# Kernel optimization log

Measured on AMD Instinct MI355X. Metric: run time of the kernel, lower is better.

The kernel has to match this reference:

```python
import jax, jax.numpy as jnp
import numpy as np

B, S, D = 2, 4096, 1024
H, DK = 16, 64          # heads, QK feature dim per head
DV = D // H             # output features per head = 64
QKV_OUT = (2 * DK + DV) * H  # 3072


def setup_inputs() -> dict:
    key = jax.random.key(0)
    k1, k2, k3, k4, k5 = jax.random.split(key, 5)
    x = jax.random.normal(k1, (B, S, D), dtype=jnp.float32)
    Wqkv = jax.random.normal(k2, (D, QKV_OUT), dtype=jnp.float32) * (1.0 / np.sqrt(D))
    bqkv = jnp.zeros((QKV_OUT,), dtype=jnp.float32)
    Wproj = jax.random.normal(k3, (D, D), dtype=jnp.float32) * (1.0 / np.sqrt(D))
    bproj = jnp.zeros((D,), dtype=jnp.float32)
    return {"x": x, "Wqkv": Wqkv, "bqkv": bqkv, "Wproj": Wproj, "bproj": bproj}


def reference(x, Wqkv, bqkv, Wproj, bproj):
    # QKV projection: [B,S,(2*DK+DV)*H]
    qkv = x @ Wqkv + bqkv
    q_len = DK * H
    Q = qkv[:, :, :q_len].reshape(B, S, H, DK).transpose(0, 2, 1, 3)        # [B,H,S,DK]
    K = qkv[:, :, q_len:2 * q_len].reshape(B, S, H, DK).transpose(0, 2, 1, 3)
    V = qkv[:, :, 2 * q_len:].reshape(B, S, H, DV).transpose(0, 2, 1, 3)    # [B,H,S,DV]

    scores = jnp.einsum("bhqd,bhkd->bhqk", Q, K) * (1.0 / np.sqrt(DK))
    # Faithful to source: causal mask is tril(ones) with zeros -> -inf,
    # i.e. +1.0 is ADDED on allowed positions (harmless constant shift per row).
    tril = jnp.tril(jnp.ones((S, S), dtype=jnp.float32))
    mask = jnp.where(tril == 0, -jnp.inf, tril)
    scores = scores + mask
    attn = jax.nn.softmax(scores, axis=-1)  # dropout disabled (p=0 / eval)

    out = jnp.einsum("bhqk,bhkd->bhqd", attn, V)            # [B,H,S,DV]
    out = out.transpose(0, 2, 1, 3).reshape(B, S, H * DV)   # [B,S,D]
    return out @ Wproj + bproj
```

## Files before the change

kernel.cpp:

```cpp
#include <hip/hip_runtime.h>
#include <stdint.h>


typedef __bf16 bf16x8 __attribute__((ext_vector_type(8)));
typedef float f32x4 __attribute__((ext_vector_type(4)));
typedef unsigned short u16x8 __attribute__((ext_vector_type(8)));
typedef unsigned short u16x4 __attribute__((ext_vector_type(4)));
typedef unsigned int u32x4 __attribute__((ext_vector_type(4)));

__device__ __forceinline__ unsigned short f2bf(float f) {
  unsigned u = __builtin_bit_cast(unsigned, f);
  u += 0x7FFFu + ((u >> 16) & 1u);
  return (unsigned short)(u >> 16);
}

__device__ __forceinline__ float fast_exp2(float x) {
#if __has_builtin(__builtin_amdgcn_exp2f)
  return __builtin_amdgcn_exp2f(x);
#else
  return exp2f(x);
#endif
}

__device__ __forceinline__ void gload16(const void* g, void* l) {
  __builtin_amdgcn_global_load_lds(
      (__attribute__((address_space(1))) unsigned int*)(uintptr_t)g,
      (__attribute__((address_space(3))) unsigned int*)(unsigned int)(uintptr_t)l,
      16, 0, 0);
}

__global__ void k_cvt_bf16(const float* __restrict__ in,
                           unsigned short* __restrict__ out, int n8) {
  int i = blockIdx.x * blockDim.x + threadIdx.x;
  if (i >= n8) return;
  const float4* p = reinterpret_cast<const float4*>(in) + (size_t)i * 2;
  float4 a = p[0], b = p[1];
  u16x8 o;
  o[0] = f2bf(a.x); o[1] = f2bf(a.y); o[2] = f2bf(a.z); o[3] = f2bf(a.w);
  o[4] = f2bf(b.x); o[5] = f2bf(b.y); o[6] = f2bf(b.z); o[7] = f2bf(b.w);
  *(reinterpret_cast<u16x8*>(out) + i) = o;
}

__global__ void k_transcvt(const float* __restrict__ in,
                           unsigned short* __restrict__ out, int K, int N) {
  __shared__ float tile[32][33];
  int tk0 = blockIdx.y << 5, tn0 = blockIdx.x << 5;
  int t = threadIdx.x;
  int r = t >> 3, c4 = (t & 7) << 2;
  float4 v = *reinterpret_cast<const float4*>(&in[(size_t)(tk0 + r) * N + tn0 + c4]);
  tile[r][c4 + 0] = v.x; tile[r][c4 + 1] = v.y;
  tile[r][c4 + 2] = v.z; tile[r][c4 + 3] = v.w;
  __syncthreads();
  u16x4 o;
  o[0] = f2bf(tile[c4 + 0][r]); o[1] = f2bf(tile[c4 + 1][r]);
  o[2] = f2bf(tile[c4 + 2][r]); o[3] = f2bf(tile[c4 + 3][r]);
  *reinterpret_cast<u16x4*>(&out[(size_t)(tn0 + r) * K + tk0 + c4]) = o;
}

__device__ __forceinline__ void gemm_core(
    const unsigned short* __restrict__ A, const unsigned short* __restrict__ Bt,
    unsigned short* Al, unsigned short* Bl, int m0, int n0, f32x4 acc[4][4]) {
  const int t = threadIdx.x;
  const int lane = t & 63;
  const int w = t >> 6;
  const int wr = w >> 1, wc = w & 1;
  const int l15 = lane & 15, l4 = lane >> 4;

  const int c0 = t, c1 = t + 256;
  const int r0 = c0 >> 2, s0 = ((c0 & 3) << 3) ^ (((r0 >> 1) & 3) << 3);
  const int r1 = c1 >> 2, s1 = ((c1 & 3) << 3) ^ (((r1 >> 1) & 3) << 3);
  const size_t ga0 = (size_t)(m0 + r0) * 1024 + s0;
  const size_t ga1 = (size_t)(m0 + r1) * 1024 + s1;
  const size_t gb0 = (size_t)(n0 + r0) * 1024 + s0;
  const size_t gb1 = (size_t)(n0 + r1) * 1024 + s1;

  int aidx[4], bidx[4];
#pragma unroll
  for (int m = 0; m < 4; ++m) {
    int row = wr * 64 + m * 16 + l15;
    aidx[m] = row * 32 + ((l4 * 8) ^ (((row >> 1) & 3) << 3));
    row = wc * 64 + m * 16 + l15;
    bidx[m] = row * 32 + ((l4 * 8) ^ (((row >> 1) & 3) << 3));
  }

  for (int kk = 0; kk < 1024; kk += 32) {
    __syncthreads();
    gload16(A + ga0 + kk, Al + c0 * 8);
    gload16(A + ga1 + kk, Al + c1 * 8);
    gload16(Bt + gb0 + kk, Bl + c0 * 8);
    gload16(Bt + gb1 + kk, Bl + c1 * 8);
    __syncthreads();
    bf16x8 af[4], bfr[4];
#pragma unroll
    for (int m = 0; m < 4; ++m)
      af[m] = *reinterpret_cast<const bf16x8*>(Al + aidx[m]);
#pragma unroll
    for (int n = 0; n < 4; ++n)
      bfr[n] = *reinterpret_cast<const bf16x8*>(Bl + bidx[n]);
#pragma unroll
    for (int m = 0; m < 4; ++m)
#pragma unroll
      for (int n = 0; n < 4; ++n)
        acc[m][n] = __builtin_amdgcn_mfma_f32_16x16x32_bf16(af[m], bfr[n],
                                                            acc[m][n], 0, 0, 0);
  }
}

__global__ __launch_bounds__(256) void k_gemm_qkv(
    const unsigned short* __restrict__ A, const unsigned short* __restrict__ Bt,
    const float* __restrict__ bias, unsigned short* __restrict__ Qb,
    unsigned short* __restrict__ Kb, unsigned short* __restrict__ VTb) {
  __shared__ unsigned short Al[128 * 32];
  __shared__ unsigned short Bl[128 * 32];
  const int lane = threadIdx.x & 63, w = threadIdx.x >> 6;
  const int wr = w >> 1, wc = w & 1;
  const int l15 = lane & 15, l4 = lane >> 4;
  const int m0 = blockIdx.y << 7, n0 = blockIdx.x << 7;
  const float C1 = 0.18033688011112043f;

  f32x4 acc[4][4] = {};
  gemm_core(A, Bt, Al, Bl, m0, n0, acc);

#pragma unroll
  for (int m = 0; m < 4; ++m) {
#pragma unroll
    for (int n = 0; n < 4; ++n) {
#pragma unroll
      for (int j = 0; j < 4; ++j) {
        int row = m0 + wr * 64 + m * 16 + l4 * 4 + j;
        int col = n0 + wc * 64 + n * 16 + l15;
        float v = acc[m][n][j] + bias[col];
        int b = row >> 12, s = row & 4095;
        if (col < 1024) {
          int hh = col >> 6, d = col & 63;
          Qb[((size_t)(b * 16 + hh) * 4096 + s) * 64 + d] = f2bf(v * C1);
        } else if (col < 2048) {
          int cc = col - 1024; int hh = cc >> 6, d = cc & 63;
          Kb[((size_t)(b * 16 + hh) * 4096 + s) * 64 + d] = f2bf(v);
        } else {
          int cc = col - 2048; int hh = cc >> 6, d = cc & 63;
          VTb[((size_t)(b * 16 + hh) * 64 + d) * 4096 + s] = f2bf(v);
        }
      }
    }
  }
}

__global__ __launch_bounds__(256) void k_gemm_proj(
    const unsigned short* __restrict__ A, const unsigned short* __restrict__ Bt,
    const float* __restrict__ bias, float* __restrict__ out) {
  __shared__ unsigned short Al[128 * 32];
  __shared__ unsigned short Bl[128 * 32];
  const int lane = threadIdx.x & 63, w = threadIdx.x >> 6;
  const int wr = w >> 1, wc = w & 1;
  const int l15 = lane & 15, l4 = lane >> 4;
  const int m0 = blockIdx.y << 7, n0 = blockIdx.x << 7;

  f32x4 acc[4][4] = {};
  gemm_core(A, Bt, Al, Bl, m0, n0, acc);

#pragma unroll
  for (int m = 0; m < 4; ++m) {
#pragma unroll
    for (int n = 0; n < 4; ++n) {
#pragma unroll
      for (int j = 0; j < 4; ++j) {
        int row = m0 + wr * 64 + m * 16 + l4 * 4 + j;
        int col = n0 + wc * 64 + n * 16 + l15;
        out[(size_t)row * 1024 + col] = acc[m][n][j] + bias[col];
      }
    }
  }
}

__global__ __launch_bounds__(256, 4) void k_attn(
    const unsigned short* __restrict__ Qb, const unsigned short* __restrict__ Kb,
    const unsigned short* __restrict__ VTb, unsigned short* __restrict__ Ob) {
  __shared__ unsigned short Kl[2][64 * 64];
  __shared__ unsigned short Vl[2][64 * 64];
  const int t = threadIdx.x;
  const int lane = t & 63, w = t >> 6;
  const int l15 = lane & 15, l4 = lane >> 4;
  const int idx = blockIdx.x;
  const int qt = 31 - (idx >> 5);
  const int bh = idx & 31;
  const size_t qkbase = (size_t)bh * 4096 * 64;
  const size_t vbase = (size_t)bh * 64 * 4096;
  const int b = bh >> 4, hh = bh & 15;
  const int wrow0 = qt * 128 + w * 32;
  const int nt = 2 * qt + 2;

  const int c0 = t, c1 = t + 256;
  const int kr0 = c0 >> 3, ks0 = ((c0 & 7) << 3) ^ ((kr0 & 7) << 3);
  const int kr1 = c1 >> 3, ks1 = ((c1 & 7) << 3) ^ ((kr1 & 7) << 3);

#define STAGE(bufi, jt)                                                             \
  do {                                                                              \
    gload16(Kb + qkbase + (size_t)((jt) * 64 + kr0) * 64 + ks0, &Kl[bufi][c0 * 8]); \
    gload16(Kb + qkbase + (size_t)((jt) * 64 + kr1) * 64 + ks1, &Kl[bufi][c1 * 8]); \
    gload16(VTb + vbase + (size_t)kr0 * 4096 + (jt) * 64 + ks0, &Vl[bufi][c0 * 8]); \
    gload16(VTb + vbase + (size_t)kr1 * 4096 + (jt) * 64 + ks1, &Vl[bufi][c1 * 8]); \
  } while (0)

  bf16x8 qf[2][2];
#pragma unroll
  for (int m = 0; m < 2; ++m)
#pragma unroll
    for (int kk = 0; kk < 2; ++kk)
      qf[m][kk] = *reinterpret_cast<const bf16x8*>(
          &Qb[qkbase + (size_t)(wrow0 + m * 16 + l15) * 64 + kk * 32 + l4 * 8]);

  f32x4 oacc[2][4] = {};
  float lsum[2] = {};

  STAGE(0, 0);
  asm volatile("s_waitcnt vmcnt(0)" ::: "memory");
  __builtin_amdgcn_s_barrier();

  for (int j = 0; j < nt; ++j) {
    const int cur = j & 1;
    if (j + 1 < nt) STAGE(cur ^ 1, j + 1);

    const int jk0 = j * 64;
    const bool active = (jk0 <= wrow0 + 31);
    const bool needmask = active && (jk0 + 63 > wrow0);

    if (active) {
#pragma unroll
      for (int h = 0; h < 2; ++h) {
        f32x4 sch[2][2] = {};
        __builtin_amdgcn_s_setprio(1);
#pragma unroll
        for (int nn = 0; nn < 2; ++nn) {
          int krow = (h * 2 + nn) * 16 + l15;
#pragma unroll
          for (int kk = 0; kk < 2; ++kk) {
            int kcol = (kk * 32 + l4 * 8) ^ ((krow & 7) << 3);
            bf16x8 kfr = *reinterpret_cast<const bf16x8*>(&Kl[cur][krow * 64 + kcol]);
#pragma unroll
            for (int m = 0; m < 2; ++m)
              sch[m][nn] = __builtin_amdgcn_mfma_f32_16x16x32_bf16(
                  kfr, qf[m][kk], sch[m][nn], 0, 0, 0);
          }
        }
        __builtin_amdgcn_s_setprio(0);

        bf16x8 pa[2];
#pragma unroll
        for (int m = 0; m < 2; ++m) {
#pragma unroll
          for (int nn = 0; nn < 2; ++nn)
#pragma unroll
            for (int r = 0; r < 4; ++r)
              sch[m][nn][r] = fast_exp2(sch[m][nn][r]);
          if (needmask) {
            const int qg = wrow0 + m * 16 + l15;
#pragma unroll
            for (int nn = 0; nn < 2; ++nn) {
              const int kb = jk0 + (h * 2 + nn) * 16 + l4 * 4;
#pragma unroll
              for (int r = 0; r < 4; ++r)
                if (kb + r > qg) sch[m][nn][r] = 0.f;
            }
          }
#pragma unroll
          for (int nn = 0; nn < 2; ++nn)
#pragma unroll
            for (int r = 0; r < 4; ++r)
              lsum[m] += sch[m][nn][r];

          unsigned A0, A1, B0, B1;
          asm("v_cvt_pk_bf16_f32 %0, %1, %2"
              : "=v"(A0) : "v"(sch[m][0][0]), "v"(sch[m][0][1]));
          asm("v_cvt_pk_bf16_f32 %0, %1, %2"
              : "=v"(A1) : "v"(sch[m][0][2]), "v"(sch[m][0][3]));
          asm("v_cvt_pk_bf16_f32 %0, %1, %2"
              : "=v"(B0) : "v"(sch[m][1][0]), "v"(sch[m][1][1]));
          asm("v_cvt_pk_bf16_f32 %0, %1, %2"
              : "=v"(B1) : "v"(sch[m][1][2]), "v"(sch[m][1][3]));
          asm("v_permlane32_swap_b32 %0, %1" : "+v"(A0), "+v"(B0));
          asm("v_permlane16_swap_b32 %0, %1" : "+v"(A0), "+v"(B0));
          asm("v_permlane32_swap_b32 %0, %1" : "+v"(A1), "+v"(B1));
          asm("v_permlane16_swap_b32 %0, %1" : "+v"(A1), "+v"(B1));
          u32x4 pw;
          pw[0] = A0; pw[1] = A1; pw[2] = B0; pw[3] = B1;
          pa[m] = __builtin_bit_cast(bf16x8, pw);
        }

        __builtin_amdgcn_s_setprio(1);
#pragma unroll
        for (int nn2 = 0; nn2 < 4; ++nn2) {
          int vr = nn2 * 16 + l15;
          int vc = (h * 32 + l4 * 8) ^ ((vr & 7) << 3);
          bf16x8 vf = *reinterpret_cast<const bf16x8*>(&Vl[cur][vr * 64 + vc]);
          oacc[0][nn2] = __builtin_amdgcn_mfma_f32_16x16x32_bf16(
              pa[0], vf, oacc[0][nn2], 0, 0, 0);
          oacc[1][nn2] = __builtin_amdgcn_mfma_f32_16x16x32_bf16(
              pa[1], vf, oacc[1][nn2], 0, 0, 0);
        }
        __builtin_amdgcn_s_setprio(0);
      }
    }

    asm volatile("s_waitcnt vmcnt(0)" ::: "memory");
    __builtin_amdgcn_s_barrier();
  }
#undef STAGE

#pragma unroll
  for (int m = 0; m < 2; ++m) {
    lsum[m] += __shfl_xor(lsum[m], 16);
    lsum[m] += __shfl_xor(lsum[m], 32);
  }
#pragma unroll
  for (int m = 0; m < 2; ++m)
#pragma unroll
    for (int jj = 0; jj < 4; ++jj) {
      float inv = 1.0f / __shfl(lsum[m], l4 * 4 + jj);
      int srow = wrow0 + m * 16 + l4 * 4 + jj;
#pragma unroll
      for (int nn = 0; nn < 4; ++nn) {
        int col = hh * 64 + nn * 16 + l15;
        Ob[((size_t)(b * 4096 + srow)) * 1024 + col] =
            __builtin_bit_cast(unsigned short, (__bf16)(oacc[m][nn][jj] * inv));
      }
    }
}

extern "C" void kernel_launch(void* const* d_in, const int* in_sizes, int n_in,
                              void* d_out, int out_size, void* d_ws, size_t ws_size,
                              hipStream_t stream) {
  const float* x = (const float*)d_in[0];
  const float* Wqkv = (const float*)d_in[1];
  const float* bqkv = (const float*)d_in[2];
  const float* Wproj = (const float*)d_in[3];
  const float* bproj = (const float*)d_in[4];

  char* ws = (char*)d_ws;
  unsigned short* xb  = (unsigned short*)(ws);
  unsigned short* Wqb = (unsigned short*)(ws + 16777216);
  unsigned short* Wpb = (unsigned short*)(ws + 23068672);
  unsigned short* Qb  = (unsigned short*)(ws + 25165824);
  unsigned short* Kb  = (unsigned short*)(ws + 41943040);
  unsigned short* VTb = (unsigned short*)(ws + 58720256);
  unsigned short* Ob  = (unsigned short*)(ws + 75497472);

  k_cvt_bf16<<<dim3(8388608 / 8 / 256), dim3(256), 0, stream>>>(x, xb, 8388608 / 8);
  k_transcvt<<<dim3(3072 / 32, 1024 / 32), dim3(256), 0, stream>>>(Wqkv, Wqb, 1024, 3072);
  k_transcvt<<<dim3(1024 / 32, 1024 / 32), dim3(256), 0, stream>>>(Wproj, Wpb, 1024, 1024);
  k_gemm_qkv<<<dim3(3072 / 128, 8192 / 128), dim3(256), 0, stream>>>(xb, Wqb, bqkv, Qb, Kb, VTb);
  k_attn<<<dim3(1024), dim3(256), 0, stream>>>(Qb, Kb, VTb, Ob);
  k_gemm_proj<<<dim3(1024 / 128, 8192 / 128), dim3(256), 0, stream>>>(Ob, Wpb, bproj, (float*)d_out);
}
```

Baseline: 222.2 us.

## Replace QKV GEMM with 256x256 tile, 4-stage LDS ring pipeline

The QKV projection GEMM moves from 128x128 tiles with 256 threads and a single-buffered LDS stage to 256x256 tiles with 512 threads and a 4-deep LDS ring. The ring prefetches three K-steps ahead using manual vmcnt waits and barriers, and the kernel raises wave priority around the MFMA bursts. The goal is more data reuse per tile and hiding global-load latency behind compute. The costs are 64KB of LDS per block, higher register pressure from 8x4 accumulators, and only 384 blocks, which may fill the CUs unevenly.

```diff
diff --git a/kernel.cpp b/kernel.cpp
--- a/kernel.cpp
+++ b/kernel.cpp
@@ -57,6 +57,139 @@
   *reinterpret_cast<u16x4*>(&out[(size_t)(tn0 + r) * K + tk0 + c4]) = o;
 }
 
+__global__ __launch_bounds__(512, 2) void k_gemm_qkv256(
+    const unsigned short* __restrict__ A, const unsigned short* __restrict__ Bt,
+    const float* __restrict__ bias, unsigned short* __restrict__ Qb,
+    unsigned short* __restrict__ Kb, unsigned short* __restrict__ VTb) {
+  __shared__ unsigned short Aring[4][8192];
+  __shared__ unsigned short Bring[4][8192];
+  const int t = threadIdx.x;
+  const int lane = t & 63;
+  const int w = t >> 6;
+  const int wr = w >> 2, wc = w & 3;
+  const int l15 = lane & 15, l4 = lane >> 4;
+  const int m0 = blockIdx.y << 8, n0 = blockIdx.x << 8;
+
+  const int ca0 = t, ca1 = t + 512;
+  const size_t gA0 = (size_t)(m0 + (ca0 & 255)) * 1024 + ((ca0 >> 8) << 3);
+  const size_t gA1 = (size_t)(m0 + (ca1 & 255)) * 1024 + ((ca1 >> 8) << 3);
+  const size_t gB0 = (size_t)(n0 + (ca0 & 255)) * 1024 + ((ca0 >> 8) << 3);
+  const size_t gB1 = (size_t)(n0 + (ca1 & 255)) * 1024 + ((ca1 >> 8) << 3);
+
+  const int abase = l4 * 2048 + (wr * 128 + l15) * 8;
+  const int bbase = l4 * 2048 + (wc * 64 + l15) * 8;
+
+  f32x4 acc[8][4] = {};
+
+  auto stageU = [&](int g) {
+    const int s = g & 3;
+    const int k = g << 5;
+    gload16(A + gA0 + k, &Aring[s][ca0 * 8]);
+    gload16(A + gA1 + k, &Aring[s][ca1 * 8]);
+    gload16(Bt + gB0 + k, &Bring[s][ca0 * 8]);
+    gload16(Bt + gB1 + k, &Bring[s][ca1 * 8]);
+  };
+
+  auto computeU = [&](int g, bool doStage) {
+    const unsigned short* As = Aring[g & 3];
+    const unsigned short* Bs = Bring[g & 3];
+    bf16x8 bfr[4], af[4];
+#pragma unroll
+    for (int nf = 0; nf < 4; ++nf)
+      bfr[nf] = *reinterpret_cast<const bf16x8*>(Bs + bbase + nf * 128);
+#pragma unroll
+    for (int mf = 0; mf < 4; ++mf)
+      af[mf] = *reinterpret_cast<const bf16x8*>(As + abase + mf * 128);
+    if (doStage) stageU(g + 3);
+    __builtin_amdgcn_s_setprio(1);
+#pragma unroll
+    for (int mf = 0; mf < 4; ++mf)
+#pragma unroll
+      for (int nf = 0; nf < 4; ++nf)
+        acc[mf][nf] = __builtin_amdgcn_mfma_f32_16x16x32_bf16(af[mf], bfr[nf],
+                                                              acc[mf][nf], 0, 0, 0);
+    __builtin_amdgcn_s_setprio(0);
+#pragma unroll
+    for (int mf = 0; mf < 4; ++mf)
+      af[mf] = *reinterpret_cast<const bf16x8*>(As + abase + 512 + mf * 128);
+    __builtin_amdgcn_s_setprio(1);
+#pragma unroll
+    for (int mf = 0; mf < 4; ++mf)
+#pragma unroll
+      for (int nf = 0; nf < 4; ++nf)
+        acc[4 + mf][nf] = __builtin_amdgcn_mfma_f32_16x16x32_bf16(
+            af[mf], bfr[nf], acc[4 + mf][nf], 0, 0, 0);
+    __builtin_amdgcn_s_setprio(0);
+  };
+
+  stageU(0); stageU(1); stageU(2);
+  asm volatile("s_waitcnt vmcnt(8)" ::: "memory");
+  asm volatile("s_barrier" ::: "memory");
+
+#pragma unroll 1
+  for (int g = 0; g < 29; ++g) {
+    computeU(g, true);
+    asm volatile("s_waitcnt vmcnt(8)" ::: "memory");
+    asm volatile("s_barrier" ::: "memory");
+  }
+  computeU(29, false);
+  asm volatile("s_waitcnt vmcnt(4)" ::: "memory");
+  asm volatile("s_barrier" ::: "memory");
+  computeU(30, false);
+  asm volatile("s_waitcnt vmcnt(0)" ::: "memory");
+  asm volatile("s_barrier" ::: "memory");
+  computeU(31, false);
+
+  const float C1 = 0.18033688011112043f;
+  float bi[4];
+#pragma unroll
+  for (int nf = 0; nf < 4; ++nf) bi[nf] = bias[n0 + wc * 64 + nf * 16 + l15];
+
+  if (n0 < 1024) {
+#pragma unroll
+    for (int amf = 0; amf < 8; ++amf)
+#pragma unroll
+      for (int nf = 0; nf < 4; ++nf)
+#pragma unroll
+        for (int j = 0; j < 4; ++j) {
+          int row = m0 + wr * 128 + amf * 16 + l4 * 4 + j;
+          int col = n0 + wc * 64 + nf * 16 + l15;
+          float v = (acc[amf][nf][j] + bi[nf]) * C1;
+          int b = row >> 12, s = row & 4095;
+          int hh = col >> 6, d = col & 63;
+          Qb[((size_t)(b * 16 + hh) * 4096 + s) * 64 + d] = f2bf(v);
+        }
+  } else if (n0 < 2048) {
+#pragma unroll
+    for (int amf = 0; amf < 8; ++amf)
+#pragma unroll
+      for (int nf = 0; nf < 4; ++nf)
+#pragma unroll
+        for (int j = 0; j < 4; ++j) {
+          int row = m0 + wr * 128 + amf * 16 + l4 * 4 + j;
+          int cc = n0 - 1024 + wc * 64 + nf * 16 + l15;
+          float v = acc[amf][nf][j] + bi[nf];
+          int b = row >> 12, s = row & 4095;
+          int hh = cc >> 6, d = cc & 63;
+          Kb[((size_t)(b * 16 + hh) * 4096 + s) * 64 + d] = f2bf(v);
+        }
+  } else {
+#pragma unroll
+    for (int amf = 0; amf < 8; ++amf)
+#pragma unroll
+      for (int nf = 0; nf < 4; ++nf)
+#pragma unroll
+        for (int j = 0; j < 4; ++j) {
+          int row = m0 + wr * 128 + amf * 16 + l4 * 4 + j;
+          int cc = n0 - 2048 + wc * 64 + nf * 16 + l15;
+          float v = acc[amf][nf][j] + bi[nf];
+          int b = row >> 12, s = row & 4095;
+          int hh = cc >> 6, d = cc & 63;
+          VTb[((size_t)(b * 16 + hh) * 64 + d) * 4096 + s] = f2bf(v);
+        }
+  }
+}
+
 __device__ __forceinline__ void gemm_core(
     const unsigned short* __restrict__ A, const unsigned short* __restrict__ Bt,
     unsigned short* Al, unsigned short* Bl, int m0, int n0, f32x4 acc[4][4]) {
@@ -103,46 +236,6 @@
       for (int n = 0; n < 4; ++n)
         acc[m][n] = __builtin_amdgcn_mfma_f32_16x16x32_bf16(af[m], bfr[n],
                                                             acc[m][n], 0, 0, 0);
-  }
-}
-
-__global__ __launch_bounds__(256) void k_gemm_qkv(
-    const unsigned short* __restrict__ A, const unsigned short* __restrict__ Bt,
-    const float* __restrict__ bias, unsigned short* __restrict__ Qb,
-    unsigned short* __restrict__ Kb, unsigned short* __restrict__ VTb) {
-  __shared__ unsigned short Al[128 * 32];
-  __shared__ unsigned short Bl[128 * 32];
-  const int lane = threadIdx.x & 63, w = threadIdx.x >> 6;
-  const int wr = w >> 1, wc = w & 1;
-  const int l15 = lane & 15, l4 = lane >> 4;
-  const int m0 = blockIdx.y << 7, n0 = blockIdx.x << 7;
-  const float C1 = 0.18033688011112043f;
-
-  f32x4 acc[4][4] = {};
-  gemm_core(A, Bt, Al, Bl, m0, n0, acc);
-
-#pragma unroll
-  for (int m = 0; m < 4; ++m) {
-#pragma unroll
-    for (int n = 0; n < 4; ++n) {
-#pragma unroll
-      for (int j = 0; j < 4; ++j) {
-        int row = m0 + wr * 64 + m * 16 + l4 * 4 + j;
-        int col = n0 + wc * 64 + n * 16 + l15;
-        float v = acc[m][n][j] + bias[col];
-        int b = row >> 12, s = row & 4095;
-        if (col < 1024) {
-          int hh = col >> 6, d = col & 63;
-          Qb[((size_t)(b * 16 + hh) * 4096 + s) * 64 + d] = f2bf(v * C1);
-        } else if (col < 2048) {
-          int cc = col - 1024; int hh = cc >> 6, d = cc & 63;
-          Kb[((size_t)(b * 16 + hh) * 4096 + s) * 64 + d] = f2bf(v);
-        } else {
-          int cc = col - 2048; int hh = cc >> 6, d = cc & 63;
-          VTb[((size_t)(b * 16 + hh) * 64 + d) * 4096 + s] = f2bf(v);
-        }
-      }
-    }
   }
 }
 
@@ -348,7 +441,7 @@
   k_cvt_bf16<<<dim3(8388608 / 8 / 256), dim3(256), 0, stream>>>(x, xb, 8388608 / 8);
   k_transcvt<<<dim3(3072 / 32, 1024 / 32), dim3(256), 0, stream>>>(Wqkv, Wqb, 1024, 3072);
   k_transcvt<<<dim3(1024 / 32, 1024 / 32), dim3(256), 0, stream>>>(Wproj, Wpb, 1024, 1024);
-  k_gemm_qkv<<<dim3(3072 / 128, 8192 / 128), dim3(256), 0, stream>>>(xb, Wqb, bqkv, Qb, Kb, VTb);
+  k_gemm_qkv256<<<dim3(3072 / 256, 8192 / 256), dim3(512), 0, stream>>>(xb, Wqb, bqkv, Qb, Kb, VTb);
   k_attn<<<dim3(1024), dim3(256), 0, stream>>>(Qb, Kb, VTb, Ob);
   k_gemm_proj<<<dim3(1024 / 128, 8192 / 128), dim3(256), 0, stream>>>(Ob, Wpb, bproj, (float*)d_out);
 }
```

After: 232.7 us. 1.05x slower.

## Double-buffer LDS tiles in GEMM core to overlap global loads with MFMA

Applied to the files above, without the earlier changes.

The shared GEMM core for the QKV and output projections now uses two LDS buffers per operand. The next K-slice is loaded directly into LDS while MFMAs run on the current slice, with one barrier per iteration instead of two. It also raises wave priority around the MFMA block. The cost is double the LDS per block, which may lower occupancy, and the vmcnt(0) wait at the end of each iteration limits how much of the load latency is hidden.

```diff
diff --git a/kernel.cpp b/kernel.cpp
--- a/kernel.cpp
+++ b/kernel.cpp
@@ -57,9 +57,10 @@
   *reinterpret_cast<u16x4*>(&out[(size_t)(tn0 + r) * K + tk0 + c4]) = o;
 }
 
-__device__ __forceinline__ void gemm_core(
+__device__ __forceinline__ void gemm_core_db(
     const unsigned short* __restrict__ A, const unsigned short* __restrict__ Bt,
-    unsigned short* Al, unsigned short* Bl, int m0, int n0, f32x4 acc[4][4]) {
+    unsigned short (*Al)[128 * 32], unsigned short (*Bl)[128 * 32],
+    int m0, int n0, f32x4 acc[4][4]) {
   const int t = threadIdx.x;
   const int lane = t & 63;
   const int w = t >> 6;
@@ -83,35 +84,49 @@
     bidx[m] = row * 32 + ((l4 * 8) ^ (((row >> 1) & 3) << 3));
   }
 
-  for (int kk = 0; kk < 1024; kk += 32) {
-    __syncthreads();
-    gload16(A + ga0 + kk, Al + c0 * 8);
-    gload16(A + ga1 + kk, Al + c1 * 8);
-    gload16(Bt + gb0 + kk, Bl + c0 * 8);
-    gload16(Bt + gb1 + kk, Bl + c1 * 8);
-    __syncthreads();
+#define GSTAGE(bufi, kofs)                                   \
+  do {                                                       \
+    gload16(A + ga0 + (kofs), Al[bufi] + c0 * 8);            \
+    gload16(A + ga1 + (kofs), Al[bufi] + c1 * 8);            \
+    gload16(Bt + gb0 + (kofs), Bl[bufi] + c0 * 8);           \
+    gload16(Bt + gb1 + (kofs), Bl[bufi] + c1 * 8);           \
+  } while (0)
+
+  GSTAGE(0, 0);
+  asm volatile("s_waitcnt vmcnt(0)" ::: "memory");
+  __builtin_amdgcn_s_barrier();
+
+#pragma unroll 1
+  for (int it = 0; it < 32; ++it) {
+    const int cur = it & 1;
+    if (it + 1 < 32) GSTAGE(cur ^ 1, (it + 1) * 32);
     bf16x8 af[4], bfr[4];
 #pragma unroll
     for (int m = 0; m < 4; ++m)
-      af[m] = *reinterpret_cast<const bf16x8*>(Al + aidx[m]);
+      af[m] = *reinterpret_cast<const bf16x8*>(Al[cur] + aidx[m]);
 #pragma unroll
     for (int n = 0; n < 4; ++n)
-      bfr[n] = *reinterpret_cast<const bf16x8*>(Bl + bidx[n]);
+      bfr[n] = *reinterpret_cast<const bf16x8*>(Bl[cur] + bidx[n]);
+    __builtin_amdgcn_s_setprio(1);
 #pragma unroll
     for (int m = 0; m < 4; ++m)
 #pragma unroll
       for (int n = 0; n < 4; ++n)
         acc[m][n] = __builtin_amdgcn_mfma_f32_16x16x32_bf16(af[m], bfr[n],
                                                             acc[m][n], 0, 0, 0);
-  }
+    __builtin_amdgcn_s_setprio(0);
+    asm volatile("s_waitcnt vmcnt(0)" ::: "memory");
+    __builtin_amdgcn_s_barrier();
+  }
+#undef GSTAGE
 }
 
 __global__ __launch_bounds__(256) void k_gemm_qkv(
     const unsigned short* __restrict__ A, const unsigned short* __restrict__ Bt,
     const float* __restrict__ bias, unsigned short* __restrict__ Qb,
     unsigned short* __restrict__ Kb, unsigned short* __restrict__ VTb) {
-  __shared__ unsigned short Al[128 * 32];
-  __shared__ unsigned short Bl[128 * 32];
+  __shared__ unsigned short Al[2][128 * 32];
+  __shared__ unsigned short Bl[2][128 * 32];
   const int lane = threadIdx.x & 63, w = threadIdx.x >> 6;
   const int wr = w >> 1, wc = w & 1;
   const int l15 = lane & 15, l4 = lane >> 4;
@@ -119,7 +134,7 @@
   const float C1 = 0.18033688011112043f;
 
   f32x4 acc[4][4] = {};
-  gemm_core(A, Bt, Al, Bl, m0, n0, acc);
+  gemm_core_db(A, Bt, Al, Bl, m0, n0, acc);
 
 #pragma unroll
   for (int m = 0; m < 4; ++m) {
@@ -149,15 +164,15 @@
 __global__ __launch_bounds__(256) void k_gemm_proj(
     const unsigned short* __restrict__ A, const unsigned short* __restrict__ Bt,
     const float* __restrict__ bias, float* __restrict__ out) {
-  __shared__ unsigned short Al[128 * 32];
-  __shared__ unsigned short Bl[128 * 32];
+  __shared__ unsigned short Al[2][128 * 32];
+  __shared__ unsigned short Bl[2][128 * 32];
   const int lane = threadIdx.x & 63, w = threadIdx.x >> 6;
   const int wr = w >> 1, wc = w & 1;
   const int l15 = lane & 15, l4 = lane >> 4;
   const int m0 = blockIdx.y << 7, n0 = blockIdx.x << 7;
 
   f32x4 acc[4][4] = {};
-  gemm_core(A, Bt, Al, Bl, m0, n0, acc);
+  gemm_core_db(A, Bt, Al, Bl, m0, n0, acc);
 
 #pragma unroll
   for (int m = 0; m < 4; ++m) {
```

Result: no change. 220.4 us (-0.8%).
